# Kernel tuning notes

Hardware: AMD Instinct MI355X
Metric: run time of the kernel (lower is better)

## Reference

```python
import jax, jax.numpy as jnp
import numpy as np

M, K, N = 4096, 4096, 11008

def setup_inputs() -> dict:
    key = jax.random.key(0)
    k1, k2, k3, k4, k5 = jax.random.split(key, 5)
    x = jax.random.normal(k1, (M, K), dtype=jnp.float32)
    # int8 weights stored as int32 carrier (values in [-128, 127])
    weight = jax.random.randint(k2, (N, K), -128, 128, dtype=jnp.int32)
    # per-channel dequant scale, small positive values
    deq_scale = jax.random.uniform(k3, (N,), dtype=jnp.float32, minval=1e-4, maxval=2e-3)
    # static per-tensor activation scale
    input_scale = jax.random.uniform(k4, (1,), dtype=jnp.float32, minval=0.02, maxval=0.05)
    input_offset = jnp.zeros((1,), dtype=jnp.int32)
    quant_bias = jax.random.randint(k5, (N,), -1000, 1000, dtype=jnp.int32)
    return {"x": x, "weight": weight, "deq_scale": deq_scale,
            "input_scale": input_scale, "input_offset": input_offset,
            "quant_bias": quant_bias}

def reference(x, weight, deq_scale, input_scale, input_offset, quant_bias):
    # Static per-tensor activation quantization to int8
    x_q = jnp.clip(jnp.round(x / input_scale) + input_offset.astype(jnp.float32),
                   -128.0, 127.0).astype(jnp.int32)  # [M, K]
    # int8 GEMM accumulated in int32 (weight stored [N, K], i.e. transposed)
    acc = jnp.einsum('mk,nk->mn', x_q, weight)  # [M, N] int32
    # add int32 quant bias, per-channel dequant to fp32
    out = (acc + quant_bias[None, :]).astype(jnp.float32) * deq_scale[None, :]
    return out
```

## Files before the change

### kernel.cpp

```cpp
#include <hip/hip_runtime.h>
#include <cstdint>
#include <cstddef>

#define M_DIM 4096
#define K_DIM 4096
#define N_DIM 11008
#define BM 128
#define BN 256
#define BKB 64
#define NT (K_DIM / BKB)
#define NTM (M_DIM / BM)
#define NTN (N_DIM / BN)
#define SLOT 24576
#define B_OFF 8192

typedef int   int4v   __attribute__((ext_vector_type(4)));
typedef float float4v __attribute__((ext_vector_type(4)));

__device__ __forceinline__ void gload_lds16(const void* g, void* l) {
  __builtin_amdgcn_global_load_lds(
      (const __attribute__((address_space(1))) unsigned int*)g,
      (__attribute__((address_space(3))) unsigned int*)l, 16, 0, 0);
}

__global__ void quant_x_kernel(const float* __restrict__ x,
                               const float* __restrict__ scale_p,
                               const int* __restrict__ off_p,
                               signed char* __restrict__ xq, int total16) {
  const float inv = 1.0f / scale_p[0];
  const float off = (float)off_p[0];
  int tid = blockIdx.x * blockDim.x + threadIdx.x;
  int stride = gridDim.x * blockDim.x;
  const float4v* x4 = (const float4v*)x;
  int4v* out4 = (int4v*)xq;
  for (int i = tid; i < total16; i += stride) {
    int4v o;
#pragma unroll
    for (int j = 0; j < 4; ++j) {
      float4v v = x4[(size_t)i * 4 + j];
      int r = 0;
#pragma unroll
      for (int e = 0; e < 4; ++e) {
        float q = rintf(v[e] * inv) + off;
        q = fminf(fmaxf(q, -128.0f), 127.0f);
        int qi = (int)q;
        r |= (qi & 0xff) << (8 * e);
      }
      o[j] = r;
    }
    out4[i] = o;
  }
}

__global__ void pack_w_kernel(const int* __restrict__ w,
                              signed char* __restrict__ wq, int total16) {
  int tid = blockIdx.x * blockDim.x + threadIdx.x;
  int stride = gridDim.x * blockDim.x;
  const int4v* w4 = (const int4v*)w;
  int4v* out4 = (int4v*)wq;
  for (int i = tid; i < total16; i += stride) {
    int4v o;
#pragma unroll
    for (int j = 0; j < 4; ++j) {
      int4v v = w4[(size_t)i * 4 + j];
      o[j] = (v[0] & 0xff) | ((v[1] & 0xff) << 8) |
             ((v[2] & 0xff) << 16) | ((v[3] & 0xff) << 24);
    }
    out4[i] = o;
  }
}

__global__ __launch_bounds__(256, 2) void gemm_i8_kernel(
    const signed char* __restrict__ A,
    const signed char* __restrict__ B,
    const int* __restrict__ qbias,
    const float* __restrict__ dscale,
    float* __restrict__ out) {
  __shared__ __attribute__((aligned(16))) signed char lds[3 * SLOT];

  const int tid  = threadIdx.x;
  const int lane = tid & 63;
  const int wv   = tid >> 6;
  const int wr   = wv >> 1;
  const int wc   = wv & 1;

  int bid = blockIdx.x;
  int s   = bid >> 3;
  int tm  = 4 * (bid & 7) + (s & 3);
  int tn  = s >> 2;

  const int csw = (((lane & 3) ^ ((lane >> 3) & 3)) << 4);
  const signed char* sA0 = A + (size_t)(tm * BM + wv * 16 + (lane >> 2)) * K_DIM + csw;
  const signed char* sB0 = B + (size_t)(tn * BN + wv * 64 + (lane >> 2)) * K_DIM + csw;
  const int dA0 = wv * 1024 + lane * 16;
  const int dB0 = B_OFF + wv * 4096 + lane * 16;

#define STG(KT, SO) do {                                                      \
    gload_lds16(sA0 + (size_t)(KT) * BKB,                    lds + (SO) + dA0);        \
    gload_lds16(sA0 + (size_t)64 * K_DIM + (size_t)(KT) * BKB, lds + (SO) + dA0 + 4096); \
    _Pragma("unroll") for (int j = 0; j < 4; ++j)                             \
      gload_lds16(sB0 + (size_t)j * 16 * K_DIM + (size_t)(KT) * BKB,          \
                  lds + (SO) + dB0 + j * 1024);                               \
  } while (0)

  const int rp  = ((((lane >> 4) ^ (lane >> 1)) & 3) << 4);
  const int rdA = (wr * 4) * 1024 + (lane & 15) * 64 + rp;
  const int rdB = B_OFF + (wc * 8) * 1024 + (lane & 15) * 64 + rp;

#define LG(n) do {                                                            \
    asm volatile("s_waitcnt lgkmcnt(" #n ")" ::: "memory");                   \
    __builtin_amdgcn_sched_barrier(0); } while (0)
#define MMH(N0) do {                                                          \
    __builtin_amdgcn_s_setprio(1);                                            \
    _Pragma("unroll") for (int m = 0; m < 4; ++m)                             \
      _Pragma("unroll") for (int n = 0; n < 4; ++n)                           \
        acc[m][(N0) + n] = __builtin_amdgcn_mfma_i32_16x16x64_i8(             \
            afr[m], bfr[(N0) + n], acc[m][(N0) + n], 0, 0, 0);                \
    __builtin_amdgcn_s_setprio(0); } while (0)

#define STEP(SB, DO_STG, KT2, S2, VMODE) do {                                 \
    _Pragma("unroll") for (int m = 0; m < 4; ++m)                             \
      afr[m] = *(const int4v*)(lds + (SB) + rdA + m * 1024);                  \
    _Pragma("unroll") for (int n = 0; n < 8; ++n)                             \
      bfr[n] = *(const int4v*)(lds + (SB) + rdB + n * 1024);                  \
    if (DO_STG) STG((KT2), (S2));                                             \
    LG(4);                                                                    \
    MMH(0);                                                                   \
    LG(0);                                                                    \
    MMH(4);                                                                   \
    if ((VMODE) == 0) { asm volatile("s_waitcnt vmcnt(6)" ::: "memory"); }    \
    else if ((VMODE) == 1) { asm volatile("s_waitcnt vmcnt(0)" ::: "memory"); } \
    if ((VMODE) != 2) __builtin_amdgcn_s_barrier();                           \
  } while (0)

  int4v acc[4][8];
#pragma unroll
  for (int i = 0; i < 4; ++i)
#pragma unroll
    for (int j = 0; j < 8; ++j) acc[i][j] = (int4v){0, 0, 0, 0};

  int4v afr[4], bfr[8];

  STG(0, 0);
  STG(1, SLOT);
  asm volatile("s_waitcnt vmcnt(6)" ::: "memory");
  __builtin_amdgcn_s_barrier();

  int c0 = 0, c1 = SLOT, c2 = 2 * SLOT;
  for (int t = 0; t < NT - 2; ++t) {
    STEP(c0, 1, t + 2, c2, 0);
    int tmp = c0; c0 = c1; c1 = c2; c2 = tmp;
  }
  STEP(c0, 0, 0, 0, 1);
  { int tmp = c0; c0 = c1; c1 = c2; c2 = tmp; }
  STEP(c0, 0, 0, 0, 2);
#undef STEP
#undef MMH
#undef LG
#undef STG

  const int col = lane & 15;
  const int rb  = (lane >> 4) * 4;
  const int gm0 = tm * BM + wr * 64;
  const int gn0 = tn * BN + wc * 128;
#pragma unroll
  for (int n = 0; n < 8; ++n) {
    int gn = gn0 + n * 16 + col;
    float ds = dscale[gn];
    int qb = qbias[gn];
#pragma unroll
    for (int m = 0; m < 4; ++m) {
      int gm = gm0 + m * 16 + rb;
#pragma unroll
      for (int j = 0; j < 4; ++j)
        out[(size_t)(gm + j) * N_DIM + gn] = (float)(acc[m][n][j] + qb) * ds;
    }
  }
}

extern "C" void kernel_launch(void* const* d_in, const int* in_sizes, int n_in,
                              void* d_out, int out_size, void* d_ws, size_t ws_size,
                              hipStream_t stream) {
  const float* x      = (const float*)d_in[0];
  const int*   w      = (const int*)d_in[1];
  const float* dscale = (const float*)d_in[2];
  const float* iscale = (const float*)d_in[3];
  const int*   ioff   = (const int*)d_in[4];
  const int*   qbias  = (const int*)d_in[5];
  float* out = (float*)d_out;

  const size_t xq_bytes = (size_t)M_DIM * K_DIM;
  const size_t wq_bytes = (size_t)N_DIM * K_DIM;
  if (ws_size < xq_bytes + wq_bytes) return;

  signed char* xq = (signed char*)d_ws;
  signed char* wq = (signed char*)d_ws + xq_bytes;

  quant_x_kernel<<<2048, 256, 0, stream>>>(x, iscale, ioff, xq, M_DIM * K_DIM / 16);
  pack_w_kernel<<<2048, 256, 0, stream>>>(w, wq, M_DIM ? N_DIM * K_DIM / 16 : 0);
  gemm_i8_kernel<<<NTM * NTN, 256, 0, stream>>>(xq, wq, qbias, dscale, out);
}
```

Measured before the change: 258.1 us.

## Split A/B LDS buffering and interleave B fragment reads with MFMAs

```diff
diff --git a/kernel.cpp b/kernel.cpp
--- a/kernel.cpp
+++ b/kernel.cpp
@@ -11,8 +11,8 @@
 #define NT (K_DIM / BKB)
 #define NTM (M_DIM / BM)
 #define NTN (N_DIM / BN)
-#define SLOT 24576
-#define B_OFF 8192
+#define A_OFF 49152
+#define ABASE(k) (A_OFF + ((k) & 3) * 8192)
 
 typedef int   int4v   __attribute__((ext_vector_type(4)));
 typedef float float4v __attribute__((ext_vector_type(4)));
@@ -76,7 +76,7 @@
     const int* __restrict__ qbias,
     const float* __restrict__ dscale,
     float* __restrict__ out) {
-  __shared__ __attribute__((aligned(16))) signed char lds[3 * SLOT];
+  __shared__ __attribute__((aligned(16))) signed char lds[81920];
 
   const int tid  = threadIdx.x;
   const int lane = tid & 63;
@@ -93,44 +93,58 @@
   const signed char* sA0 = A + (size_t)(tm * BM + wv * 16 + (lane >> 2)) * K_DIM + csw;
   const signed char* sB0 = B + (size_t)(tn * BN + wv * 64 + (lane >> 2)) * K_DIM + csw;
   const int dA0 = wv * 1024 + lane * 16;
-  const int dB0 = B_OFF + wv * 4096 + lane * 16;
-
-#define STG(KT, SO) do {                                                      \
-    gload_lds16(sA0 + (size_t)(KT) * BKB,                    lds + (SO) + dA0);        \
-    gload_lds16(sA0 + (size_t)64 * K_DIM + (size_t)(KT) * BKB, lds + (SO) + dA0 + 4096); \
+  const int dB0 = wv * 4096 + lane * 16;
+
+#define STG_A(KT, AB) do {                                                    \
+    gload_lds16(sA0 + (size_t)(KT) * BKB,                      lds + (AB) + dA0);        \
+    gload_lds16(sA0 + (size_t)64 * K_DIM + (size_t)(KT) * BKB, lds + (AB) + dA0 + 4096); \
+  } while (0)
+#define STG_B(KT, SBX) do {                                                   \
     _Pragma("unroll") for (int j = 0; j < 4; ++j)                             \
       gload_lds16(sB0 + (size_t)j * 16 * K_DIM + (size_t)(KT) * BKB,          \
-                  lds + (SO) + dB0 + j * 1024);                               \
+                  lds + (SBX) + dB0 + j * 1024);                              \
   } while (0)
 
   const int rp  = ((((lane >> 4) ^ (lane >> 1)) & 3) << 4);
-  const int rdA = (wr * 4) * 1024 + (lane & 15) * 64 + rp;
-  const int rdB = B_OFF + (wc * 8) * 1024 + (lane & 15) * 64 + rp;
-
-#define LG(n) do {                                                            \
+  const int rdo = (lane & 15) * 64 + rp;
+  const int rdA = (wr * 4) * 1024 + rdo;
+  const int rdB = (wc * 8) * 1024 + rdo;
+
+#define RD_B(SBX, n) (*(const int4v*)(lds + (SBX) + rdB + (n) * 1024))
+#define RD_A4(DST, AB) do {                                                   \
+    _Pragma("unroll") for (int m = 0; m < 4; ++m)                             \
+      DST[m] = *(const int4v*)(lds + (AB) + rdA + m * 1024); } while (0)
+
+#define LGSB(n) do {                                                          \
     asm volatile("s_waitcnt lgkmcnt(" #n ")" ::: "memory");                   \
     __builtin_amdgcn_sched_barrier(0); } while (0)
-#define MMH(N0) do {                                                          \
+#define MMG(AC, BR, NI) do {                                                  \
     __builtin_amdgcn_s_setprio(1);                                            \
     _Pragma("unroll") for (int m = 0; m < 4; ++m)                             \
-      _Pragma("unroll") for (int n = 0; n < 4; ++n)                           \
-        acc[m][(N0) + n] = __builtin_amdgcn_mfma_i32_16x16x64_i8(             \
-            afr[m], bfr[(N0) + n], acc[m][(N0) + n], 0, 0, 0);                \
+      acc[m][NI] = __builtin_amdgcn_mfma_i32_16x16x64_i8(                     \
+          AC[m], BR, acc[m][NI], 0, 0, 0);                                    \
     __builtin_amdgcn_s_setprio(0); } while (0)
 
-#define STEP(SB, DO_STG, KT2, S2, VMODE) do {                                 \
-    _Pragma("unroll") for (int m = 0; m < 4; ++m)                             \
-      afr[m] = *(const int4v*)(lds + (SB) + rdA + m * 1024);                  \
-    _Pragma("unroll") for (int n = 0; n < 8; ++n)                             \
-      bfr[n] = *(const int4v*)(lds + (SB) + rdB + n * 1024);                  \
-    if (DO_STG) STG((KT2), (S2));                                             \
-    LG(4);                                                                    \
-    MMH(0);                                                                   \
-    LG(0);                                                                    \
-    MMH(4);                                                                   \
-    if ((VMODE) == 0) { asm volatile("s_waitcnt vmcnt(6)" ::: "memory"); }    \
-    else if ((VMODE) == 1) { asm volatile("s_waitcnt vmcnt(0)" ::: "memory"); } \
-    if ((VMODE) != 2) __builtin_amdgcn_s_barrier();                           \
+#define STEP(T, AC, AN, LAST) do {                                            \
+    int kA_ = ((T) + 3) & (NT - 1);                                           \
+    int kB_ = ((T) + 2) & (NT - 1);                                           \
+    STG_A(kA_, ABASE(kA_));                                                   \
+    STG_B(kB_, sb2);                                                          \
+    br0 = RD_B(sb0, 0); br1 = RD_B(sb0, 1); br2 = RD_B(sb0, 2);               \
+    LGSB(2); MMG(AC, br0, 0); br0 = RD_B(sb0, 3);                             \
+    LGSB(2); MMG(AC, br1, 1); br1 = RD_B(sb0, 4);                             \
+    LGSB(2); MMG(AC, br2, 2); br2 = RD_B(sb0, 5);                             \
+    LGSB(2); MMG(AC, br0, 3); br0 = RD_B(sb0, 6);                             \
+    LGSB(2); MMG(AC, br1, 4); br1 = RD_B(sb0, 7);                             \
+    LGSB(2); MMG(AC, br2, 5);                                                 \
+    if (!(LAST)) { RD_A4(AN, ABASE((T) + 1)); }                               \
+    if (LAST) { LGSB(1); } else { LGSB(5); }                                  \
+    MMG(AC, br0, 6);                                                          \
+    if (LAST) { LGSB(0); } else { LGSB(4); }                                  \
+    MMG(AC, br1, 7);                                                          \
+    asm volatile("s_waitcnt vmcnt(6)" ::: "memory");                          \
+    __builtin_amdgcn_s_barrier();                                             \
+    int _r = sb0; sb0 = sb1; sb1 = sb2; sb2 = _r;                             \
   } while (0)
 
   int4v acc[4][8];
@@ -139,25 +153,29 @@
 #pragma unroll
     for (int j = 0; j < 8; ++j) acc[i][j] = (int4v){0, 0, 0, 0};
 
-  int4v afr[4], bfr[8];
-
-  STG(0, 0);
-  STG(1, SLOT);
-  asm volatile("s_waitcnt vmcnt(6)" ::: "memory");
+  int4v Aev[4], Aod[4], br0, br1, br2;
+  int sb0 = 0, sb1 = 16384, sb2 = 32768;
+
+  STG_A(0, ABASE(0)); STG_A(1, ABASE(1)); STG_A(2, ABASE(2));
+  STG_B(0, 0); STG_B(1, 16384);
+  asm volatile("s_waitcnt vmcnt(4)" ::: "memory");
   __builtin_amdgcn_s_barrier();
-
-  int c0 = 0, c1 = SLOT, c2 = 2 * SLOT;
-  for (int t = 0; t < NT - 2; ++t) {
-    STEP(c0, 1, t + 2, c2, 0);
-    int tmp = c0; c0 = c1; c1 = c2; c2 = tmp;
-  }
-  STEP(c0, 0, 0, 0, 1);
-  { int tmp = c0; c0 = c1; c1 = c2; c2 = tmp; }
-  STEP(c0, 0, 0, 0, 2);
+  RD_A4(Aev, ABASE(0));
+
+  for (int t = 0; t < NT - 2; t += 2) {
+    STEP(t,     Aev, Aod, 0);
+    STEP(t + 1, Aod, Aev, 0);
+  }
+  STEP(NT - 2, Aev, Aod, 0);
+  STEP(NT - 1, Aod, Aev, 1);
+  asm volatile("s_waitcnt vmcnt(0) lgkmcnt(0)" ::: "memory");
 #undef STEP
-#undef MMH
-#undef LG
-#undef STG
+#undef MMG
+#undef LGSB
+#undef RD_A4
+#undef RD_B
+#undef STG_B
+#undef STG_A
 
   const int col = lane & 15;
   const int rb  = (lane >> 4) * 4;
@@ -197,6 +215,6 @@
   signed char* wq = (signed char*)d_ws + xq_bytes;
 
   quant_x_kernel<<<2048, 256, 0, stream>>>(x, iscale, ioff, xq, M_DIM * K_DIM / 16);
-  pack_w_kernel<<<2048, 256, 0, stream>>>(w, wq, M_DIM ? N_DIM * K_DIM / 16 : 0);
+  pack_w_kernel<<<2048, 256, 0, stream>>>(w, wq, N_DIM * K_DIM / 16);
   gemm_i8_kernel<<<NTM * NTN, 256, 0, stream>>>(xq, wq, qbias, dscale, out);
 }
```

Result: no change. 262.7 us (+1.8%).

## Double-buffer register fragments to overlap LDS reads with MFMA

Applied to the files above, without the earlier changes.

```diff
diff --git a/kernel.cpp b/kernel.cpp
--- a/kernel.cpp
+++ b/kernel.cpp
@@ -107,30 +107,29 @@
   const int rdA = (wr * 4) * 1024 + (lane & 15) * 64 + rp;
   const int rdB = B_OFF + (wc * 8) * 1024 + (lane & 15) * 64 + rp;
 
-#define LG(n) do {                                                            \
-    asm volatile("s_waitcnt lgkmcnt(" #n ")" ::: "memory");                   \
-    __builtin_amdgcn_sched_barrier(0); } while (0)
-#define MMH(N0) do {                                                          \
+#define RD(AF, BF, SB) do {                                                   \
+    _Pragma("unroll") for (int m = 0; m < 4; ++m)                             \
+      AF[m] = *(const int4v*)(lds + (SB) + rdA + m * 1024);                   \
+    _Pragma("unroll") for (int n = 0; n < 8; ++n)                             \
+      BF[n] = *(const int4v*)(lds + (SB) + rdB + n * 1024); } while (0)
+
+#define MM(AF, BF) do {                                                       \
     __builtin_amdgcn_s_setprio(1);                                            \
     _Pragma("unroll") for (int m = 0; m < 4; ++m)                             \
-      _Pragma("unroll") for (int n = 0; n < 4; ++n)                           \
-        acc[m][(N0) + n] = __builtin_amdgcn_mfma_i32_16x16x64_i8(             \
-            afr[m], bfr[(N0) + n], acc[m][(N0) + n], 0, 0, 0);                \
+      _Pragma("unroll") for (int n = 0; n < 8; ++n)                           \
+        acc[m][n] = __builtin_amdgcn_mfma_i32_16x16x64_i8(                    \
+            AF[m], BF[n], acc[m][n], 0, 0, 0);                                \
     __builtin_amdgcn_s_setprio(0); } while (0)
 
-#define STEP(SB, DO_STG, KT2, S2, VMODE) do {                                 \
-    _Pragma("unroll") for (int m = 0; m < 4; ++m)                             \
-      afr[m] = *(const int4v*)(lds + (SB) + rdA + m * 1024);                  \
-    _Pragma("unroll") for (int n = 0; n < 8; ++n)                             \
-      bfr[n] = *(const int4v*)(lds + (SB) + rdB + n * 1024);                  \
-    if (DO_STG) STG((KT2), (S2));                                             \
-    LG(4);                                                                    \
-    MMH(0);                                                                   \
-    LG(0);                                                                    \
-    MMH(4);                                                                   \
-    if ((VMODE) == 0) { asm volatile("s_waitcnt vmcnt(6)" ::: "memory"); }    \
-    else if ((VMODE) == 1) { asm volatile("s_waitcnt vmcnt(0)" ::: "memory"); } \
-    if ((VMODE) != 2) __builtin_amdgcn_s_barrier();                           \
+#define STEP(KT2, CUR_A, CUR_B, NXT_A, NXT_B) do {                            \
+    STG((KT2) & (NT - 1), c2);                                                \
+    RD(NXT_A, NXT_B, c1);                                                     \
+    MM(CUR_A, CUR_B);                                                         \
+    asm volatile("s_waitcnt lgkmcnt(0)" ::: "memory");                        \
+    __builtin_amdgcn_sched_barrier(0);                                        \
+    asm volatile("s_waitcnt vmcnt(0)" ::: "memory");                          \
+    __builtin_amdgcn_s_barrier();                                             \
+    int _r = c0; c0 = c1; c1 = c2; c2 = _r;                                   \
   } while (0)
 
   int4v acc[4][8];
@@ -139,24 +138,24 @@
 #pragma unroll
     for (int j = 0; j < 8; ++j) acc[i][j] = (int4v){0, 0, 0, 0};
 
-  int4v afr[4], bfr[8];
+  int4v afrE[4], bfrE[8], afrO[4], bfrO[8];
+  int c0 = 0, c1 = SLOT, c2 = 2 * SLOT;
 
   STG(0, 0);
   STG(1, SLOT);
-  asm volatile("s_waitcnt vmcnt(6)" ::: "memory");
+  asm volatile("s_waitcnt vmcnt(0)" ::: "memory");
   __builtin_amdgcn_s_barrier();
-
-  int c0 = 0, c1 = SLOT, c2 = 2 * SLOT;
-  for (int t = 0; t < NT - 2; ++t) {
-    STEP(c0, 1, t + 2, c2, 0);
-    int tmp = c0; c0 = c1; c1 = c2; c2 = tmp;
-  }
-  STEP(c0, 0, 0, 0, 1);
-  { int tmp = c0; c0 = c1; c1 = c2; c2 = tmp; }
-  STEP(c0, 0, 0, 0, 2);
+  RD(afrE, bfrE, 0);
+  asm volatile("s_waitcnt lgkmcnt(0)" ::: "memory");
+  __builtin_amdgcn_sched_barrier(0);
+
+  for (int t = 0; t < NT; t += 2) {
+    STEP(t + 2, afrE, bfrE, afrO, bfrO);
+    STEP(t + 3, afrO, bfrO, afrE, bfrE);
+  }
 #undef STEP
-#undef MMH
-#undef LG
+#undef MM
+#undef RD
 #undef STG
 
   const int col = lane & 15;
@@ -197,6 +196,6 @@
   signed char* wq = (signed char*)d_ws + xq_bytes;
 
   quant_x_kernel<<<2048, 256, 0, stream>>>(x, iscale, ioff, xq, M_DIM * K_DIM / 16);
-  pack_w_kernel<<<2048, 256, 0, stream>>>(w, wq, M_DIM ? N_DIM * K_DIM / 16 : 0);
+  pack_w_kernel<<<2048, 256, 0, stream>>>(w, wq, N_DIM * K_DIM / 16);
   gemm_i8_kernel<<<NTM * NTN, 256, 0, stream>>>(xq, wq, qbias, dscale, out);
 }
```

Result: slower. 264.6 us (+2.5%).
